# Performance work log

Hardware: AMD Instinct MI355X
Metric: run time of the kernel (lower is better)

## Reference

```python
import jax, jax.numpy as jnp
import numpy as np

D_MODEL = 4096
N_HEADS = 32
N_KV_HEADS = 32
D_HEAD = 128
D_LATENT = 512
N_CKV = 4            # n_compressed_kv_heads = d_latent // d_head
T = 2048             # num_tokens (single-sequence prefill)
ROPE_BASE = 10000.0
NEG = -1e30


def _rope(x, positions):
    """Neox-style rotary embedding. x: (T, H, D)."""
    d = x.shape[-1]
    inv_freq = 1.0 / (ROPE_BASE ** (jnp.arange(0, d // 2, dtype=jnp.float32) * (2.0 / d)))
    freqs = positions.astype(jnp.float32)[:, None] * inv_freq[None, :]  # (T, D/2)
    cos = jnp.cos(freqs)[:, None, :]
    sin = jnp.sin(freqs)[:, None, :]
    x1, x2 = jnp.split(x, 2, axis=-1)
    return jnp.concatenate([x1 * cos - x2 * sin, x2 * cos + x1 * sin], axis=-1)


def setup_inputs() -> dict:
    key = jax.random.key(0)
    ks = jax.random.split(key, 6)
    s = jnp.float32(0.02)
    return {
        "positions": jnp.arange(T, dtype=jnp.int32),
        "hidden_states": jax.random.normal(ks[0], (T, D_MODEL), jnp.float32),
        "Wq": jax.random.normal(ks[1], (D_MODEL, N_HEADS * D_HEAD), jnp.float32) * s,
        "Wc": jax.random.normal(ks[2], (D_MODEL, 2 * D_LATENT), jnp.float32) * s,
        "Wuk": jax.random.normal(ks[3], (2 * D_LATENT, N_KV_HEADS * D_HEAD), jnp.float32) * s,
        "Wuv": jax.random.normal(ks[4], (2 * D_LATENT, N_KV_HEADS * D_HEAD), jnp.float32) * s,
        "Wo": jax.random.normal(ks[5], (N_HEADS * D_HEAD, D_MODEL), jnp.float32) * s,
    }


def reference(positions, hidden_states, Wq, Wc, Wuk, Wuv, Wo):
    # Q projection
    q = (hidden_states @ Wq).reshape(T, N_HEADS, D_HEAD)
    # MLA compression: hidden -> c_kv (2*d_latent), split into c_k / c_v
    c_kv = hidden_states @ Wc                                   # (T, 2*D_LATENT)
    c_k = c_kv[:, :D_LATENT].reshape(T, N_CKV, D_HEAD)          # compressed K cache
    c_v = c_kv[:, D_LATENT:].reshape(T, N_CKV, D_HEAD)          # compressed V cache
    # Decompression (computed by the source module; K is RoPE'd then discarded,
    # V is unused -- the v1 attention path runs over the compressed cache).
    K = (c_kv @ Wuk).reshape(T, N_KV_HEADS, D_HEAD)
    V = (c_kv @ Wuv).reshape(T, N_KV_HEADS, D_HEAD)             # noqa: unused, matches source
    # RoPE on q (and K, whose rotated value is dead in the source)
    q = _rope(q, positions)
    K = _rope(K, positions)  # dead, kept for FLOP parity with the source
    # GQA attention: n_heads=32 query heads over n_compressed_kv_heads=4 kv heads
    g = N_HEADS // N_CKV
    qg = q.reshape(T, N_CKV, g, D_HEAD)
    scale = jnp.float32(1.0 / np.sqrt(D_HEAD))
    scores = jnp.einsum('tkgd,skd->kgts', qg, c_k) * scale      # (N_CKV, g, T, T)
    causal = positions[:, None] >= positions[None, :]           # (T, T)
    scores = jnp.where(causal[None, None], scores, NEG)
    probs = jax.nn.softmax(scores, axis=-1)
    ctx = jnp.einsum('kgts,skd->tkgd', probs, c_v).reshape(T, N_HEADS * D_HEAD)
    return ctx @ Wo
```

## Files before the change

kernel.cpp:

```cpp
#include <hip/hip_runtime.h>
#include <hip/hip_bf16.h>
#include <cstdint>
#include <cstddef>


typedef unsigned short u16;
typedef short s16x8 __attribute__((ext_vector_type(8)));
typedef short s16x4 __attribute__((ext_vector_type(4)));
typedef float f32x4 __attribute__((ext_vector_type(4)));

#define MFMA16(a, b, c) __builtin_amdgcn_mfma_f32_16x16x32_bf16((a), (b), (c), 0, 0, 0)

#define QSCALE 0.12751899f
#define LOG2_ROPE_BASE 13.287712379549449f
#define FIXMAX 24.0f

__device__ __forceinline__ u16 f2b(float f) {
  return __builtin_bit_cast(u16, __float2bfloat16(f));
}
__device__ __forceinline__ void async_copy16(u16* lds, const u16* g) {
  __builtin_amdgcn_global_load_lds(
      (const __attribute__((address_space(1))) unsigned int*)g,
      (__attribute__((address_space(3))) unsigned int*)lds, 16, 0, 0);
}

__global__ __launch_bounds__(256)
void prep_kernel(const float* __restrict__ hidden, const float* __restrict__ Wq,
                 const float* __restrict__ Wc, const float* __restrict__ Wo,
                 u16* __restrict__ hb, u16* __restrict__ WqT,
                 u16* __restrict__ WcT, u16* __restrict__ WoT) {
  __shared__ alignas(16) u16 tile[64 * 72];
  const int b = blockIdx.x;
  const int t = threadIdx.x;

  if (b >= 9216) {
    int i = (b - 9216) * 256 + t;
    const float4* p = (const float4*)hidden + (size_t)i * 2;
    float4 a = p[0], c = p[1];
    s16x8 v;
    v[0] = (short)f2b(a.x); v[1] = (short)f2b(a.y);
    v[2] = (short)f2b(a.z); v[3] = (short)f2b(a.w);
    v[4] = (short)f2b(c.x); v[5] = (short)f2b(c.y);
    v[6] = (short)f2b(c.z); v[7] = (short)f2b(c.w);
    *(s16x8*)&hb[(size_t)i * 8] = v;
    return;
  }

  const float* in;
  u16* out;
  int gx, in_ld, out_ld;
  if (b < 4096)      { in = Wq; out = WqT; gx = b;        in_ld = 4096; out_ld = 4096; }
  else if (b < 5120) { in = Wc; out = WcT; gx = b - 4096; in_ld = 1024; out_ld = 4096; }
  else               { in = Wo; out = WoT; gx = b - 5120; in_ld = 4096; out_ld = 4096; }
  const int nbx = in_ld / 64;
  const int c0 = (gx % nbx) * 64, r0 = (gx / nbx) * 64;
  const int rr = t >> 3, cc = (t & 7) * 8;
#pragma unroll
  for (int p = 0; p < 2; p++) {
    int row = p * 32 + rr;
    const float4* src = (const float4*)&in[(size_t)(r0 + row) * in_ld + c0 + cc];
    float4 a = src[0], c = src[1];
    s16x8 v;
    v[0] = (short)f2b(a.x); v[1] = (short)f2b(a.y);
    v[2] = (short)f2b(a.z); v[3] = (short)f2b(a.w);
    v[4] = (short)f2b(c.x); v[5] = (short)f2b(c.y);
    v[6] = (short)f2b(c.z); v[7] = (short)f2b(c.w);
    *(s16x8*)&tile[row * 72 + cc] = v;
  }
  __syncthreads();
#pragma unroll
  for (int p = 0; p < 2; p++) {
    int orow = p * 32 + rr;
    s16x8 v;
#pragma unroll
    for (int j = 0; j < 8; j++) v[j] = (short)tile[(cc + j) * 72 + orow];
    *(s16x8*)&out[(size_t)(c0 + orow) * out_ld + r0 + cc] = v;
  }
}

__global__ __launch_bounds__(256)
void transpose_ckv(const u16* __restrict__ in, u16* __restrict__ out) {
  __shared__ alignas(16) u16 tile[64 * 72];
  const int kh = blockIdx.z;
  const int c0 = blockIdx.x * 64, r0 = blockIdx.y * 64;
  const int in_off = 512 + kh * 128;
  u16* outk = out + (size_t)kh * 128 * 2048;
  const int t = threadIdx.x;
  const int rr = t >> 3, cc = (t & 7) * 8;
#pragma unroll
  for (int p = 0; p < 2; p++) {
    int row = p * 32 + rr;
    s16x8 v = *(const s16x8*)&in[(size_t)(r0 + row) * 1024 + in_off + c0 + cc];
    *(s16x8*)&tile[row * 72 + cc] = v;
  }
  __syncthreads();
#pragma unroll
  for (int p = 0; p < 2; p++) {
    int orow = p * 32 + rr;
    s16x8 v;
#pragma unroll
    for (int j = 0; j < 8; j++) v[j] = (short)tile[(cc + j) * 72 + orow];
    *(s16x8*)&outk[(size_t)(c0 + orow) * 2048 + r0 + cc] = v;
  }
}

template <int EPI>
__global__ __launch_bounds__(256, 3)
void gemm_bt(const u16* __restrict__ A, const u16* __restrict__ Bt,
             void* __restrict__ Cv, void* __restrict__ Cv2,
             const int* __restrict__ positions) {
  __shared__ alignas(16) u16 As[2][128 * 32];
  __shared__ alignas(16) u16 Bs[2][128 * 32];

  const int tid = threadIdx.x;
  const int w = tid >> 6, l = tid & 63;
  const int wm = w >> 1, wn = w & 1;
  const int lrow = l >> 4, lcol = l & 15;
  const int m0 = blockIdx.y * 128, n0 = blockIdx.x * 128;

  f32x4 acc[4][4] = {};

  const int srow = l >> 2;
  const int scol = (l & 3) * 8;
  const u16* Ag = A + (size_t)(m0 + w * 32 + srow) * 4096 + scol;
  const u16* Bg = Bt + (size_t)(n0 + w * 32 + srow) * 4096 + scol;

  for (int kt = 0; kt < 4096; kt += 64) {
    __syncthreads();
#pragma unroll
    for (int hf = 0; hf < 2; hf++) {
      async_copy16(&As[hf][(w * 32) * 32], Ag + kt + hf * 32);
      async_copy16(&As[hf][(w * 32 + 16) * 32],
                   Ag + (size_t)16 * 4096 + kt + hf * 32);
      async_copy16(&Bs[hf][(w * 32) * 32], Bg + kt + hf * 32);
      async_copy16(&Bs[hf][(w * 32 + 16) * 32],
                   Bg + (size_t)16 * 4096 + kt + hf * 32);
    }
    __syncthreads();

#pragma unroll
    for (int hf = 0; hf < 2; hf++) {
      s16x8 a[4], b[4];
#pragma unroll
      for (int i = 0; i < 4; i++)
        a[i] = *(const s16x8*)&As[hf][(wm * 64 + i * 16 + lcol) * 32 + lrow * 8];
#pragma unroll
      for (int j = 0; j < 4; j++)
        b[j] = *(const s16x8*)&Bs[hf][(wn * 32 + (j & 1) * 16 + (j >> 1) * 64 +
                                       lcol) * 32 + lrow * 8];
#pragma unroll
      for (int i = 0; i < 4; i++)
#pragma unroll
        for (int j = 0; j < 4; j++)
          acc[i][j] = MFMA16(a[i], b[j], acc[i][j]);
    }
  }

  if constexpr (EPI == 3) {
    float* C = (float*)Cv;
#pragma unroll
    for (int i = 0; i < 4; i++) {
      int row = m0 + wm * 64 + i * 16 + lrow * 4;
#pragma unroll
      for (int j = 0; j < 4; j++) {
        int col = n0 + wn * 32 + (j & 1) * 16 + (j >> 1) * 64 + lcol;
#pragma unroll
        for (int r = 0; r < 4; r++)
          C[(size_t)(row + r) * 4096 + col] = acc[i][j][r];
      }
    }
  } else {
    if (n0 >= 4096) {
      u16* C = (u16*)Cv2;
      int cb = n0 - 4096;
#pragma unroll
      for (int i = 0; i < 4; i++) {
        int row = m0 + wm * 64 + i * 16 + lrow * 4;
#pragma unroll
        for (int j = 0; j < 4; j++) {
          int col = cb + wn * 32 + (j & 1) * 16 + (j >> 1) * 64 + lcol;
#pragma unroll
          for (int r = 0; r < 4; r++)
            C[(size_t)(row + r) * 1024 + col] = f2b(acc[i][j][r]);
        }
      }
    } else {
      u16* C = (u16*)Cv;
      float inv[2];
#pragma unroll
      for (int j = 0; j < 2; j++) {
        int d = wn * 32 + j * 16 + lcol;
        inv[j] = exp2f((float)d * (-LOG2_ROPE_BASE / 64.f));
      }
#pragma unroll
      for (int i = 0; i < 4; i++) {
        int row = m0 + wm * 64 + i * 16 + lrow * 4;
#pragma unroll
        for (int r = 0; r < 4; r++) {
          float pos = (float)positions[row + r];
#pragma unroll
          for (int j = 0; j < 2; j++) {
            int d = wn * 32 + j * 16 + lcol;
            float ang = pos * inv[j];
            float sv, cv;
            sincosf(ang, &sv, &cv);
            float x1 = acc[i][j][r];
            float x2 = acc[i][j + 2][r];
            C[(size_t)(row + r) * 4096 + n0 + d] = f2b((x1 * cv - x2 * sv) * QSCALE);
            C[(size_t)(row + r) * 4096 + n0 + d + 64] =
                f2b((x2 * cv + x1 * sv) * QSCALE);
          }
        }
      }
    }
  }
}

__global__ __launch_bounds__(256)
void attn_kernel(const u16* __restrict__ Q, const u16* __restrict__ ckv,
                 const u16* __restrict__ vT, u16* __restrict__ ctx) {
  __shared__ alignas(16) u16 Kt[2][8192];
  __shared__ alignas(16) u16 Vt[2][8192];
  __shared__ alignas(16) u16 Ps[4][4096];
  __shared__ alignas(16) float red[4][32];

  const int tid = threadIdx.x, w = tid >> 6, l = tid & 63;
  const int lrow = l >> 4, lcol = l & 15;
  const int h = blockIdx.y, kh = h >> 3;
  const int q0w = w * 32;
  const int sxor = (l >> 3) & 3;
  const int kxor = (lcol >> 1) & 3;

  const u16* kg0 = ckv + (size_t)(w * 16 + (l >> 2)) * 1024 + kh * 128 +
                   (((l & 3) ^ sxor)) * 8;
  const u16* vg0 = vT + (size_t)(kh * 128 + w * 32 + (l >> 2)) * 2048 +
                   (((l & 3) ^ sxor)) * 8;

#pragma unroll 1
  for (int qi = 0; qi < 2; qi++) {
    const int qt = qi ? (int)blockIdx.x : 15 - (int)blockIdx.x;

    s16x8 qf[2][4];
    {
      const u16* qg =
          Q + (size_t)(qt * 128 + q0w + lcol) * 4096 + h * 128 + lrow * 8;
#pragma unroll
      for (int nt = 0; nt < 2; nt++)
#pragma unroll
        for (int kc = 0; kc < 4; kc++)
          qf[nt][kc] = *(const s16x8*)&qg[(size_t)(nt * 16) * 4096 + kc * 32];
    }

    f32x4 o[2][8] = {};
    float l_run[2] = {0.f, 0.f};
    const int nkt = 2 * (qt + 1);

    {
      const u16* kg = kg0;
#pragma unroll
      for (int kc = 0; kc < 4; kc++)
        async_copy16(&Kt[0][kc * 2048 + (w * 16) * 32], kg + kc * 32);
      const u16* vg = vg0;
#pragma unroll
      for (int kc = 0; kc < 2; kc++) {
        async_copy16(&Vt[0][kc * 4096 + (w * 32) * 32], vg + kc * 32);
        async_copy16(&Vt[0][kc * 4096 + (w * 32 + 16) * 32],
                     vg + (size_t)16 * 2048 + kc * 32);
      }
    }
    asm volatile("s_waitcnt vmcnt(0)" ::: "memory");
    __syncthreads();

#pragma unroll 1
    for (int kt = 0; kt < nkt; kt++) {
      const int cur = kt & 1;
      if (kt + 1 < nkt) {
        const u16* kg = kg0 + (size_t)(kt + 1) * 64 * 1024;
#pragma unroll
        for (int kc = 0; kc < 4; kc++)
          async_copy16(&Kt[cur ^ 1][kc * 2048 + (w * 16) * 32], kg + kc * 32);
        const u16* vg = vg0 + (size_t)(kt + 1) * 64;
#pragma unroll
        for (int kc = 0; kc < 2; kc++) {
          async_copy16(&Vt[cur ^ 1][kc * 4096 + (w * 32) * 32], vg + kc * 32);
          async_copy16(&Vt[cur ^ 1][kc * 4096 + (w * 32 + 16) * 32],
                       vg + (size_t)16 * 2048 + kc * 32);
        }
      }

      f32x4 s[4][2] = {};
#pragma unroll
      for (int kc = 0; kc < 4; kc++)
#pragma unroll
        for (int mt = 0; mt < 4; mt++) {
          s16x8 ka = *(const s16x8*)&Kt[cur][kc * 2048 + (mt * 16 + lcol) * 32 +
                                            (lrow ^ kxor) * 8];
          s[mt][0] = MFMA16(ka, qf[0][kc], s[mt][0]);
          s[mt][1] = MFMA16(ka, qf[1][kc], s[mt][1]);
        }

      if (kt >= 2 * qt) {
        int koff = (kt & 1) * 64;
#pragma unroll
        for (int mt = 0; mt < 4; mt++)
#pragma unroll
          for (int nt = 0; nt < 2; nt++)
#pragma unroll
            for (int r = 0; r < 4; r++) {
              int key = koff + mt * 16 + lrow * 4 + r;
              int q = q0w + nt * 16 + lcol;
              if (key > q) s[mt][nt][r] = -1e30f;
            }
      }

#pragma unroll
      for (int nt = 0; nt < 2; nt++) {
        float sum = 0.f;
#pragma unroll
        for (int mt = 0; mt < 4; mt++) {
          s16x4 pk;
#pragma unroll
          for (int r = 0; r < 4; r++) {
            float p = exp2f(s[mt][nt][r] - FIXMAX);
            sum += p;
            pk[r] = (short)f2b(p);
          }
          int key = mt * 16 + lrow * 4;
          *(s16x4*)&Ps[w][(key >> 5) * 2048 + (nt * 16 + lcol) * 32 +
                          ((key & 31) ^ (kxor << 3))] = pk;
        }
        sum += __shfl_xor(sum, 16);
        sum += __shfl_xor(sum, 32);
        l_run[nt] += sum;
      }

#pragma unroll
      for (int kc = 0; kc < 2; kc++) {
        s16x8 pa0 = *(const s16x8*)&Ps[w][kc * 2048 + lcol * 32 +
                                          (lrow ^ kxor) * 8];
        s16x8 pa1 = *(const s16x8*)&Ps[w][kc * 2048 + (16 + lcol) * 32 +
                                          (lrow ^ kxor) * 8];
#pragma unroll
        for (int ntO = 0; ntO < 8; ntO++) {
          s16x8 vb = *(const s16x8*)&Vt[cur][kc * 4096 + (ntO * 16 + lcol) * 32 +
                                             (lrow ^ kxor) * 8];
          o[0][ntO] = MFMA16(pa0, vb, o[0][ntO]);
          o[1][ntO] = MFMA16(pa1, vb, o[1][ntO]);
        }
      }

      asm volatile("s_waitcnt vmcnt(0)" ::: "memory");
      __syncthreads();
    }

    if (l < 16) {
      red[w][l] = 1.f / l_run[0];
      red[w][16 + l] = 1.f / l_run[1];
    }
    __syncthreads();
    f32x4 lf0 = *(const f32x4*)&red[w][lrow * 4];
    f32x4 lf1 = *(const f32x4*)&red[w][16 + lrow * 4];
#pragma unroll
    for (int mtO = 0; mtO < 2; mtO++)
#pragma unroll
      for (int ntO = 0; ntO < 8; ntO++)
#pragma unroll
        for (int r = 0; r < 4; r++) {
          float lv = mtO ? lf1[r] : lf0[r];
          int q = qt * 128 + q0w + mtO * 16 + lrow * 4 + r;
          int d = h * 128 + ntO * 16 + lcol;
          ctx[(size_t)q * 4096 + d] = f2b(o[mtO][ntO][r] * lv);
        }
    __syncthreads();
  }
}

extern "C" void kernel_launch(void* const* d_in, const int* in_sizes, int n_in,
                              void* d_out, int out_size, void* d_ws, size_t ws_size,
                              hipStream_t stream) {
  const int* positions = (const int*)d_in[0];
  const float* hidden = (const float*)d_in[1];
  const float* Wq = (const float*)d_in[2];
  const float* Wc = (const float*)d_in[3];
  const float* Wo = (const float*)d_in[6];

  char* ws = (char*)d_ws;
  u16* hb  = (u16*)(ws);
  u16* WT  = (u16*)(ws + 16777216);
  u16* qbf = (u16*)(ws + 58720256);
  u16* ckv = (u16*)(ws + 75497472);
  u16* cvT = (u16*)(ws + 79691776);
  u16* WoT = (u16*)(ws + 81788928);
  u16* ctx = hb;

  dim3 blk(256);

  prep_kernel<<<dim3(13312), blk, 0, stream>>>(hidden, Wq, Wc, Wo, hb, WT,
                                               WT + (size_t)4096 * 4096, WoT);

  gemm_bt<1><<<dim3(40, 16), blk, 0, stream>>>(hb, WT, qbf, ckv, positions);

  transpose_ckv<<<dim3(2, 32, 4), blk, 0, stream>>>(ckv, cvT);

  attn_kernel<<<dim3(8, 32), blk, 0, stream>>>(qbf, ckv, cvT, ctx);

  gemm_bt<3><<<dim3(32, 16), blk, 0, stream>>>(ctx, WoT, d_out, nullptr,
                                               positions);
}
```

Baseline: 482.8 us.

## Repartition attention so each block handles four heads sharing one KV head

Changes the attention work decomposition. Each block now covers a 32-query tile for four query heads that share one compressed KV head (one head per wave), where before it covered 128 queries of a single head. This cuts redundant K/V tile loads across heads in a group and raises the block count to 512 for better load balance, with causal tiles paired for balance. It also shrinks the P scratch buffer, processes P·V in two 32-key panels, adds s_setprio around the MFMA sections, and requests two blocks per CU. The risk is more blocks each doing less work per K/V tile, and higher register pressure under the new launch bound.

Result: faster. 465.7 us (-3.6%).

```diff
diff --git a/kernel.cpp b/kernel.cpp
--- a/kernel.cpp
+++ b/kernel.cpp
@@ -216,163 +216,158 @@
   }
 }
 
-__global__ __launch_bounds__(256)
+__global__ __launch_bounds__(256, 2)
 void attn_kernel(const u16* __restrict__ Q, const u16* __restrict__ ckv,
                  const u16* __restrict__ vT, u16* __restrict__ ctx) {
   __shared__ alignas(16) u16 Kt[2][8192];
   __shared__ alignas(16) u16 Vt[2][8192];
-  __shared__ alignas(16) u16 Ps[4][4096];
-  __shared__ alignas(16) float red[4][32];
+  __shared__ alignas(16) u16 Ps[4][1024];
 
   const int tid = threadIdx.x, w = tid >> 6, l = tid & 63;
   const int lrow = l >> 4, lcol = l & 15;
-  const int h = blockIdx.y, kh = h >> 3;
-  const int q0w = w * 32;
+  const int b = blockIdx.x;
+  const int hg = b & 7;
+  const int qi = b >> 3;
+  const int qt = (qi < 32) ? qi : 95 - qi;
+  const int kh = hg >> 1;
+  const int h = hg * 4 + w;
+  const int nkt = (qt >> 1) + 1;
   const int sxor = (l >> 3) & 3;
   const int kxor = (lcol >> 1) & 3;
 
   const u16* kg0 = ckv + (size_t)(w * 16 + (l >> 2)) * 1024 + kh * 128 +
-                   (((l & 3) ^ sxor)) * 8;
+                   ((l & 3) ^ sxor) * 8;
   const u16* vg0 = vT + (size_t)(kh * 128 + w * 32 + (l >> 2)) * 2048 +
-                   (((l & 3) ^ sxor)) * 8;
+                   ((l & 3) ^ sxor) * 8;
+
+  s16x8 qf[2][4];
+  {
+    const u16* qg = Q + (size_t)(qt * 32 + lcol) * 4096 + h * 128 + lrow * 8;
+#pragma unroll
+    for (int nt = 0; nt < 2; nt++)
+#pragma unroll
+      for (int kc = 0; kc < 4; kc++)
+        qf[nt][kc] = *(const s16x8*)&qg[(size_t)(nt * 16) * 4096 + kc * 32];
+  }
+
+  f32x4 o[2][8] = {};
+  float l_run[2] = {0.f, 0.f};
+
+  {
+#pragma unroll
+    for (int kc = 0; kc < 4; kc++)
+      async_copy16(&Kt[0][kc * 2048 + (w * 16) * 32], kg0 + kc * 32);
+#pragma unroll
+    for (int kc = 0; kc < 2; kc++) {
+      async_copy16(&Vt[0][kc * 4096 + (w * 32) * 32], vg0 + kc * 32);
+      async_copy16(&Vt[0][kc * 4096 + (w * 32 + 16) * 32],
+                   vg0 + (size_t)16 * 2048 + kc * 32);
+    }
+  }
+  asm volatile("s_waitcnt vmcnt(0)" ::: "memory");
+  __syncthreads();
 
 #pragma unroll 1
-  for (int qi = 0; qi < 2; qi++) {
-    const int qt = qi ? (int)blockIdx.x : 15 - (int)blockIdx.x;
-
-    s16x8 qf[2][4];
-    {
-      const u16* qg =
-          Q + (size_t)(qt * 128 + q0w + lcol) * 4096 + h * 128 + lrow * 8;
+  for (int kt = 0; kt < nkt; kt++) {
+    const int cur = kt & 1;
+    if (kt + 1 < nkt) {
+      const u16* kg = kg0 + (size_t)(kt + 1) * 64 * 1024;
+#pragma unroll
+      for (int kc = 0; kc < 4; kc++)
+        async_copy16(&Kt[cur ^ 1][kc * 2048 + (w * 16) * 32], kg + kc * 32);
+      const u16* vg = vg0 + (size_t)(kt + 1) * 64;
+#pragma unroll
+      for (int kc = 0; kc < 2; kc++) {
+        async_copy16(&Vt[cur ^ 1][kc * 4096 + (w * 32) * 32], vg + kc * 32);
+        async_copy16(&Vt[cur ^ 1][kc * 4096 + (w * 32 + 16) * 32],
+                     vg + (size_t)16 * 2048 + kc * 32);
+      }
+    }
+
+    f32x4 s[4][2] = {};
+    __builtin_amdgcn_s_setprio(1);
+#pragma unroll
+    for (int kc = 0; kc < 4; kc++)
+#pragma unroll
+      for (int mt = 0; mt < 4; mt++) {
+        s16x8 ka = *(const s16x8*)&Kt[cur][kc * 2048 + (mt * 16 + lcol) * 32 +
+                                          (lrow ^ kxor) * 8];
+        s[mt][0] = MFMA16(ka, qf[0][kc], s[mt][0]);
+        s[mt][1] = MFMA16(ka, qf[1][kc], s[mt][1]);
+      }
+    __builtin_amdgcn_s_setprio(0);
+
+    if (kt == nkt - 1) {
+      const int qoff = (qt & 1) * 32;
+#pragma unroll
+      for (int mt = 0; mt < 4; mt++)
+#pragma unroll
+        for (int nt = 0; nt < 2; nt++)
+#pragma unroll
+          for (int r = 0; r < 4; r++) {
+            int key = mt * 16 + lrow * 4 + r;
+            int q = qoff + nt * 16 + lcol;
+            if (key > q) s[mt][nt][r] = -1e30f;
+          }
+    }
+
+#pragma unroll
+    for (int pan = 0; pan < 2; pan++) {
 #pragma unroll
       for (int nt = 0; nt < 2; nt++)
 #pragma unroll
-        for (int kc = 0; kc < 4; kc++)
-          qf[nt][kc] = *(const s16x8*)&qg[(size_t)(nt * 16) * 4096 + kc * 32];
-    }
-
-    f32x4 o[2][8] = {};
-    float l_run[2] = {0.f, 0.f};
-    const int nkt = 2 * (qt + 1);
-
-    {
-      const u16* kg = kg0;
-#pragma unroll
-      for (int kc = 0; kc < 4; kc++)
-        async_copy16(&Kt[0][kc * 2048 + (w * 16) * 32], kg + kc * 32);
-      const u16* vg = vg0;
-#pragma unroll
-      for (int kc = 0; kc < 2; kc++) {
-        async_copy16(&Vt[0][kc * 4096 + (w * 32) * 32], vg + kc * 32);
-        async_copy16(&Vt[0][kc * 4096 + (w * 32 + 16) * 32],
-                     vg + (size_t)16 * 2048 + kc * 32);
-      }
-    }
+        for (int mi = 0; mi < 2; mi++) {
+          const int mt = pan * 2 + mi;
+          s16x4 pk;
+#pragma unroll
+          for (int r = 0; r < 4; r++) {
+            float p = exp2f(s[mt][nt][r] - FIXMAX);
+            l_run[nt] += p;
+            pk[r] = (short)f2b(p);
+          }
+          const int key32 = mi * 16 + lrow * 4;
+          *(s16x4*)&Ps[w][(nt * 16 + lcol) * 32 + (key32 ^ (kxor << 3))] = pk;
+        }
+      s16x8 pa0 = *(const s16x8*)&Ps[w][lcol * 32 + (lrow ^ kxor) * 8];
+      s16x8 pa1 = *(const s16x8*)&Ps[w][(16 + lcol) * 32 + (lrow ^ kxor) * 8];
+      __builtin_amdgcn_s_setprio(1);
+#pragma unroll
+      for (int ntO = 0; ntO < 8; ntO++) {
+        s16x8 vb = *(const s16x8*)&Vt[cur][pan * 4096 + (ntO * 16 + lcol) * 32 +
+                                           (lrow ^ kxor) * 8];
+        o[0][ntO] = MFMA16(pa0, vb, o[0][ntO]);
+        o[1][ntO] = MFMA16(pa1, vb, o[1][ntO]);
+      }
+      __builtin_amdgcn_s_setprio(0);
+    }
+
     asm volatile("s_waitcnt vmcnt(0)" ::: "memory");
     __syncthreads();
-
-#pragma unroll 1
-    for (int kt = 0; kt < nkt; kt++) {
-      const int cur = kt & 1;
-      if (kt + 1 < nkt) {
-        const u16* kg = kg0 + (size_t)(kt + 1) * 64 * 1024;
-#pragma unroll
-        for (int kc = 0; kc < 4; kc++)
-          async_copy16(&Kt[cur ^ 1][kc * 2048 + (w * 16) * 32], kg + kc * 32);
-        const u16* vg = vg0 + (size_t)(kt + 1) * 64;
-#pragma unroll
-        for (int kc = 0; kc < 2; kc++) {
-          async_copy16(&Vt[cur ^ 1][kc * 4096 + (w * 32) * 32], vg + kc * 32);
-          async_copy16(&Vt[cur ^ 1][kc * 4096 + (w * 32 + 16) * 32],
-                       vg + (size_t)16 * 2048 + kc * 32);
-        }
-      }
-
-      f32x4 s[4][2] = {};
-#pragma unroll
-      for (int kc = 0; kc < 4; kc++)
-#pragma unroll
-        for (int mt = 0; mt < 4; mt++) {
-          s16x8 ka = *(const s16x8*)&Kt[cur][kc * 2048 + (mt * 16 + lcol) * 32 +
-                                            (lrow ^ kxor) * 8];
-          s[mt][0] = MFMA16(ka, qf[0][kc], s[mt][0]);
-          s[mt][1] = MFMA16(ka, qf[1][kc], s[mt][1]);
-        }
-
-      if (kt >= 2 * qt) {
-        int koff = (kt & 1) * 64;
-#pragma unroll
-        for (int mt = 0; mt < 4; mt++)
-#pragma unroll
-          for (int nt = 0; nt < 2; nt++)
-#pragma unroll
-            for (int r = 0; r < 4; r++) {
-              int key = koff + mt * 16 + lrow * 4 + r;
-              int q = q0w + nt * 16 + lcol;
-              if (key > q) s[mt][nt][r] = -1e30f;
-            }
-      }
-
-#pragma unroll
-      for (int nt = 0; nt < 2; nt++) {
-        float sum = 0.f;
-#pragma unroll
-        for (int mt = 0; mt < 4; mt++) {
-          s16x4 pk;
-#pragma unroll
-          for (int r = 0; r < 4; r++) {
-            float p = exp2f(s[mt][nt][r] - FIXMAX);
-            sum += p;
-            pk[r] = (short)f2b(p);
-          }
-          int key = mt * 16 + lrow * 4;
-          *(s16x4*)&Ps[w][(key >> 5) * 2048 + (nt * 16 + lcol) * 32 +
-                          ((key & 31) ^ (kxor << 3))] = pk;
-        }
-        sum += __shfl_xor(sum, 16);
-        sum += __shfl_xor(sum, 32);
-        l_run[nt] += sum;
-      }
-
-#pragma unroll
-      for (int kc = 0; kc < 2; kc++) {
-        s16x8 pa0 = *(const s16x8*)&Ps[w][kc * 2048 + lcol * 32 +
-                                          (lrow ^ kxor) * 8];
-        s16x8 pa1 = *(const s16x8*)&Ps[w][kc * 2048 + (16 + lcol) * 32 +
-                                          (lrow ^ kxor) * 8];
-#pragma unroll
-        for (int ntO = 0; ntO < 8; ntO++) {
-          s16x8 vb = *(const s16x8*)&Vt[cur][kc * 4096 + (ntO * 16 + lcol) * 32 +
-                                             (lrow ^ kxor) * 8];
-          o[0][ntO] = MFMA16(pa0, vb, o[0][ntO]);
-          o[1][ntO] = MFMA16(pa1, vb, o[1][ntO]);
-        }
-      }
-
-      asm volatile("s_waitcnt vmcnt(0)" ::: "memory");
-      __syncthreads();
-    }
-
-    if (l < 16) {
-      red[w][l] = 1.f / l_run[0];
-      red[w][16 + l] = 1.f / l_run[1];
-    }
-    __syncthreads();
-    f32x4 lf0 = *(const f32x4*)&red[w][lrow * 4];
-    f32x4 lf1 = *(const f32x4*)&red[w][16 + lrow * 4];
-#pragma unroll
-    for (int mtO = 0; mtO < 2; mtO++)
-#pragma unroll
-      for (int ntO = 0; ntO < 8; ntO++)
-#pragma unroll
-        for (int r = 0; r < 4; r++) {
-          float lv = mtO ? lf1[r] : lf0[r];
-          int q = qt * 128 + q0w + mtO * 16 + lrow * 4 + r;
-          int d = h * 128 + ntO * 16 + lcol;
-          ctx[(size_t)q * 4096 + d] = f2b(o[mtO][ntO][r] * lv);
-        }
-    __syncthreads();
-  }
+  }
+
+#pragma unroll
+  for (int nt = 0; nt < 2; nt++) {
+    l_run[nt] += __shfl_xor(l_run[nt], 16);
+    l_run[nt] += __shfl_xor(l_run[nt], 32);
+  }
+  float* fl = (float*)&Ps[w][0];
+  if (l < 16) {
+    fl[l] = 1.f / l_run[0];
+    fl[16 + l] = 1.f / l_run[1];
+  }
+  f32x4 lf0 = *(const f32x4*)&fl[lrow * 4];
+  f32x4 lf1 = *(const f32x4*)&fl[16 + lrow * 4];
+#pragma unroll
+  for (int mtO = 0; mtO < 2; mtO++)
+#pragma unroll
+    for (int ntO = 0; ntO < 8; ntO++)
+#pragma unroll
+      for (int r = 0; r < 4; r++) {
+        float lv = mtO ? lf1[r] : lf0[r];
+        int q = qt * 32 + mtO * 16 + lrow * 4 + r;
+        int d = h * 128 + ntO * 16 + lcol;
+        ctx[(size_t)q * 4096 + d] = f2b(o[mtO][ntO][r] * lv);
+      }
 }
 
 extern "C" void kernel_launch(void* const* d_in, const int* in_sizes, int n_in,
@@ -402,7 +397,7 @@
 
   transpose_ckv<<<dim3(2, 32, 4), blk, 0, stream>>>(ckv, cvT);
 
-  attn_kernel<<<dim3(8, 32), blk, 0, stream>>>(qbf, ckv, cvT, ctx);
+  attn_kernel<<<dim3(512), blk, 0, stream>>>(qbf, ckv, cvT, ctx);
 
   gemm_bt<3><<<dim3(32, 16), blk, 0, stream>>>(ctx, WoT, d_out, nullptr,
                                                positions);
```
